# Kernel optimization log

Hardware: AMD Instinct MI355X
Metric: run time of the kernel (lower is better)

Reference implementation:

```python
import jax, jax.numpy as jnp
import numpy as np

N_NODES = 50000
N_EDGES = 800000
IN_C, OUT_C, EDGE_F, HEADS, HID, FINAL = 8, 16, 8, 4, 64, 128
NEG_SLOPE = 0.2  # PyG GATConv default LeakyReLU slope


def setup_inputs() -> dict:
    key = jax.random.key(0)
    ks = jax.random.split(key, 12)
    s = 0.1
    return {
        "x": jax.random.normal(ks[0], (N_NODES, IN_C), jnp.float32),
        "edge_index": jax.random.randint(ks[1], (2, N_EDGES), 0, N_NODES, jnp.int64),
        "edge_attr": jax.random.normal(ks[2], (N_EDGES, EDGE_F), jnp.float32),
        # NNConv params: root weight, bias, edge-MLP Linear(EDGE_F -> IN_C*OUT_C)
        "ecc_root": jax.random.normal(ks[3], (IN_C, OUT_C), jnp.float32) * s,
        "ecc_bias": jnp.zeros((OUT_C,), jnp.float32),
        "mlp_w": jax.random.normal(ks[4], (EDGE_F, IN_C * OUT_C), jnp.float32) * s,
        "mlp_b": jnp.zeros((IN_C * OUT_C,), jnp.float32),
        # GATConv params
        "gat_lin": jax.random.normal(ks[5], (OUT_C, HEADS * HID), jnp.float32) * s,
        "att_src": jax.random.normal(ks[6], (HEADS, HID), jnp.float32) * s,
        "att_dst": jax.random.normal(ks[7], (HEADS, HID), jnp.float32) * s,
        "gat_bias": jnp.zeros((HEADS * HID,), jnp.float32),
        # final Linear
        "fc_w": jax.random.normal(ks[8], (HEADS * HID, FINAL), jnp.float32) * s,
        "fc_b": jnp.zeros((FINAL,), jnp.float32),
    }


def _forward(x, edge_index, edge_attr, ecc_root, ecc_bias, mlp_w, mlp_b,
             gat_lin, att_src, att_dst, gat_bias, fc_w, fc_b):
    src, dst = edge_index[0], edge_index[1]  # messages flow src -> dst

    # ---- NNConv (edge-conditioned conv), aggr='add' ----
    # per-edge weight matrices [E, IN_C, OUT_C] from edge MLP
    w_e = (edge_attr @ mlp_w + mlp_b).reshape(-1, IN_C, OUT_C)
    msg = jnp.einsum('ei,eio->eo', x[src], w_e)                 # [E, OUT_C]
    agg = jax.ops.segment_sum(msg, dst, num_segments=N_NODES)   # [N, OUT_C]
    h = jax.nn.relu(x @ ecc_root + agg + ecc_bias)              # [N, OUT_C]

    # ---- GATConv (heads concatenated) ----
    g = (h @ gat_lin).reshape(N_NODES, HEADS, HID)              # [N, H, D]
    a_src = jnp.einsum('nhd,hd->nh', g, att_src)                # [N, H]
    a_dst = jnp.einsum('nhd,hd->nh', g, att_dst)
    e = jax.nn.leaky_relu(a_src[src] + a_dst[dst], NEG_SLOPE)   # [E, H]
    # segment softmax over incoming edges of each dst node
    e_max = jax.ops.segment_max(e, dst, num_segments=N_NODES)   # [N, H]
    e_max = jnp.where(jnp.isfinite(e_max), e_max, 0.0)
    e_exp = jnp.exp(e - e_max[dst])                             # [E, H]
    denom = jax.ops.segment_sum(e_exp, dst, num_segments=N_NODES)
    alpha = e_exp / (denom[dst] + 1e-16)                        # [E, H]
    out = jax.ops.segment_sum(alpha[:, :, None] * g[src], dst,
                              num_segments=N_NODES)             # [N, H, D]
    out = jax.nn.relu(out.reshape(N_NODES, HEADS * HID) + gat_bias)

    # ---- final linear ----
    return out @ fc_w + fc_b                                    # [N, FINAL]


def reference(x, edge_index, edge_attr, ecc_root, ecc_bias, mlp_w, mlp_b,
              gat_lin, att_src, att_dst, gat_bias, fc_w, fc_b):
    return _forward(x, edge_index, edge_attr, ecc_root, ecc_bias, mlp_w, mlp_b,
                    gat_lin, att_src, att_dst, gat_bias, fc_w, fc_b)
```

## Files before the change

kernel.cpp:

```cpp
#include <hip/hip_runtime.h>

#define N_NODES 50000
#define N_EDGES 800000
#define IN_C 8
#define OUT_C 16
#define EDGE_F 8
#define HEADS 4
#define HID 64
#define GDIM (HEADS*HID)
#define FINAL 128
#define NEG_SLOPE 0.2f
#define EB ((N_EDGES+255)/256)
#define NBLK 196

__device__ __forceinline__ int clampn(int v) {
    return v < 0 ? 0 : (v >= N_NODES ? N_NODES - 1 : v);
}

__global__ __launch_bounds__(256) void k_histfold(
    const int* __restrict__ dst, int* __restrict__ cnt, int* __restrict__ rnk,
    const float* __restrict__ gat_lin,
    const float* __restrict__ att_src_w, const float* __restrict__ att_dst_w,
    float* __restrict__ wsrc, float* __restrict__ wdst)
{
    if (blockIdx.x < EB) {
        int e = blockIdx.x * 256 + threadIdx.x;
        if (e >= N_EDGES) return;
        rnk[e] = atomicAdd(&cnt[clampn(dst[e])], 1);
    } else {
        int t = threadIdx.x;
        if (t >= 64) return;
        int c = t >> 2, h = t & 3;
        float ws = 0.f, wd = 0.f;
        for (int k = 0; k < HID; k++) {
            float l = gat_lin[c * GDIM + h * HID + k];
            ws += l * att_src_w[h * HID + k];
            wd += l * att_dst_w[h * HID + k];
        }
        wsrc[t] = ws;
        wdst[t] = wd;
    }
}

__global__ __launch_bounds__(256) void k_part(const int* __restrict__ cnt,
                                              int* __restrict__ part)
{
    int i = blockIdx.x * 256 + threadIdx.x;
    int v = (i < N_NODES) ? cnt[i] : 0;
#pragma unroll
    for (int off = 32; off; off >>= 1) v += __shfl_down(v, off);
    __shared__ int ws[4];
    if ((threadIdx.x & 63) == 0) ws[threadIdx.x >> 6] = v;
    __syncthreads();
    if (threadIdx.x == 0) part[blockIdx.x] = ws[0] + ws[1] + ws[2] + ws[3];
}

__global__ __launch_bounds__(256) void k_scan1(const int* __restrict__ part,
                                               int* __restrict__ partscan)
{
    int t = threadIdx.x;
    int v = (t < NBLK) ? part[t] : 0;
    int lane = t & 63, wid = t >> 6;
    int incl = v;
#pragma unroll
    for (int off = 1; off < 64; off <<= 1) {
        int u = __shfl_up(incl, off);
        if (lane >= off) incl += u;
    }
    __shared__ int wsum[4];
    if (lane == 63) wsum[wid] = incl;
    __syncthreads();
    int add = 0;
    for (int w = 0; w < wid; w++) add += wsum[w];
    partscan[t] = incl - v + add;
}

__global__ __launch_bounds__(256) void k_add(const int* __restrict__ cnt,
                                             const int* __restrict__ partscan,
                                             int* __restrict__ offs)
{
    int i = blockIdx.x * 256 + threadIdx.x;
    int v = (i < N_NODES) ? cnt[i] : 0;
    int lane = threadIdx.x & 63, wid = threadIdx.x >> 6;
    int incl = v;
#pragma unroll
    for (int off = 1; off < 64; off <<= 1) {
        int u = __shfl_up(incl, off);
        if (lane >= off) incl += u;
    }
    __shared__ int wsum[4];
    if (lane == 63) wsum[wid] = incl;
    __syncthreads();
    int add = partscan[blockIdx.x];
    for (int w = 0; w < wid; w++) add += wsum[w];
    if (i < N_NODES) offs[i] = incl - v + add;
    if (i == 0) offs[N_NODES] = N_EDGES;
}

__global__ __launch_bounds__(256) void k_scatter(
    const int* __restrict__ src, const int* __restrict__ dst,
    const int* __restrict__ rnk, const int* __restrict__ offs,
    int2* __restrict__ se_csr)
{
    int e = blockIdx.x * 256 + threadIdx.x;
    if (e >= N_EDGES) return;
    int p = offs[clampn(dst[e])] + rnk[e];
    se_csr[p] = make_int2(clampn(src[e]), e);
}

__global__ __launch_bounds__(256) void k2T_wave(
    const float* __restrict__ x,
    const int2* __restrict__ se_csr, const int* __restrict__ offs,
    const float* __restrict__ ea,
    const float* __restrict__ mlp_w, const float* __restrict__ mlp_b,
    const float* __restrict__ ecc_root, const float* __restrict__ ecc_bias,
    const float* __restrict__ wsrc, const float* __restrict__ wdst,
    float* __restrict__ h_tab, float* __restrict__ asrc, float* __restrict__ adst)
{
    __shared__ float smW[64 * 17];
    __shared__ float smb[128];
    __shared__ float sroot[128];
    __shared__ float sbias[16];
    __shared__ float sws[64], swd[64];
    __shared__ float sT[4][64];
    __shared__ float sxs[4][8];

    int t = threadIdx.x;
    for (int idx = t; idx < 1024; idx += 256)
        smW[(idx >> 4) * 17 + (idx & 15)] = mlp_w[idx];
    if (t < 128) smb[t] = mlp_b[t];
    if (t >= 128 && t < 256) sroot[t - 128] = ecc_root[t - 128];
    if (t < 16) sbias[t] = ecc_bias[t];
    if (t >= 32 && t < 96) sws[t - 32] = wsrc[t - 32];
    if (t >= 96 && t < 160) swd[t - 96] = wdst[t - 96];

    int wid = t >> 6, lane = t & 63;
    int n = blockIdx.x * 4 + wid;
    int f = lane >> 3, i = lane & 7;
    int beg = offs[n], end = offs[n + 1];

    float t0 = 0.f, t1 = 0.f, t2 = 0.f, t3 = 0.f, xs = 0.f;
    int j = beg;
    for (; j + 3 < end; j += 4) {
        int2 se0 = se_csr[j],     se1 = se_csr[j + 1];
        int2 se2 = se_csr[j + 2], se3 = se_csr[j + 3];
        float a0 = ea[(size_t)se0.y * EDGE_F + f];
        float a1 = ea[(size_t)se1.y * EDGE_F + f];
        float a2 = ea[(size_t)se2.y * EDGE_F + f];
        float a3 = ea[(size_t)se3.y * EDGE_F + f];
        float x0 = x[se0.x * IN_C + i];
        float x1 = x[se1.x * IN_C + i];
        float x2 = x[se2.x * IN_C + i];
        float x3 = x[se3.x * IN_C + i];
        t0 += a0 * x0; t1 += a1 * x1; t2 += a2 * x2; t3 += a3 * x3;
        xs += (x0 + x1) + (x2 + x3);
    }
    for (; j < end; j++) {
        int2 se = se_csr[j];
        float a = ea[(size_t)se.y * EDGE_F + f];
        float xv = x[se.x * IN_C + i];
        t0 += a * xv;
        xs += xv;
    }
    sT[wid][lane] = (t0 + t1) + (t2 + t3);
    if (f == 0) sxs[wid][i] = xs;
    __syncthreads();

    int o = lane & 15, p = lane >> 4;
    float v = 0.f;
#pragma unroll
    for (int q2 = 0; q2 < 16; q2++) {
        int jj = p * 16 + q2;
        v += smW[jj * 17 + o] * sT[wid][jj];
    }
    v += __shfl_down(v, 32);
    v += __shfl_down(v, 16);

    float hv = 0.f;
    if (lane < 16) {
        float vv = v + sbias[o];
#pragma unroll
        for (int ii = 0; ii < IN_C; ii++) {
            vv += smb[ii * 16 + o] * sxs[wid][ii];
            vv += x[n * IN_C + ii] * sroot[ii * 16 + o];
        }
        hv = fmaxf(vv, 0.f);
        h_tab[n * OUT_C + o] = hv;
    }
    float as = 0.f, ad = 0.f;
    int h2 = lane & 3;
#pragma unroll
    for (int c = 0; c < 16; c++) {
        float hc = __shfl(hv, c);
        as += hc * sws[c * 4 + h2];
        ad += hc * swd[c * 4 + h2];
    }
    if (lane < 4) {
        asrc[n * HEADS + lane] = as;
        adst[n * HEADS + lane] = ad;
    }
}

__global__ __launch_bounds__(256) void k_gatE(
    const int* __restrict__ offs, const int2* __restrict__ se_csr,
    const float* __restrict__ asrc, const float* __restrict__ adst,
    const float* __restrict__ h_tab, float* __restrict__ U_all)
{
    int t = threadIdx.x;
    int wid = t >> 6, lane = t & 63;
    int n = blockIdx.x * 4 + wid;
    int h = lane >> 4, c = lane & 15;
    float adsth = adst[n * HEADS + h];
    int beg = offs[n], end = offs[n + 1];

    float U = 0.f, den = 0.f;
    int j = beg;
    for (; j + 3 < end; j += 4) {
        int s0 = se_csr[j].x,     s1 = se_csr[j + 1].x;
        int s2 = se_csr[j + 2].x, s3 = se_csr[j + 3].x;
        float av0 = asrc[s0 * HEADS + h], av1 = asrc[s1 * HEADS + h];
        float av2 = asrc[s2 * HEADS + h], av3 = asrc[s3 * HEADS + h];
        float h0 = h_tab[s0 * OUT_C + c], h1 = h_tab[s1 * OUT_C + c];
        float h2v = h_tab[s2 * OUT_C + c], h3v = h_tab[s3 * OUT_C + c];
        float v0 = av0 + adsth; v0 = v0 > 0.f ? v0 : NEG_SLOPE * v0;
        float v1 = av1 + adsth; v1 = v1 > 0.f ? v1 : NEG_SLOPE * v1;
        float v2 = av2 + adsth; v2 = v2 > 0.f ? v2 : NEG_SLOPE * v2;
        float v3 = av3 + adsth; v3 = v3 > 0.f ? v3 : NEG_SLOPE * v3;
        float p0 = __expf(v0), p1 = __expf(v1), p2 = __expf(v2), p3 = __expf(v3);
        den += (p0 + p1) + (p2 + p3);
        U += p0 * h0 + p1 * h1 + p2 * h2v + p3 * h3v;
    }
    for (; j < end; j++) {
        int s = se_csr[j].x;
        float av = asrc[s * HEADS + h];
        float hvv = h_tab[s * OUT_C + c];
        float v = av + adsth; v = v > 0.f ? v : NEG_SLOPE * v;
        float pe = __expf(v);
        den += pe;
        U += pe * hvv;
    }
    U_all[(size_t)n * 64 + lane] = U / (den + 1e-16f);
}

#define FBM 32
__global__ __launch_bounds__(256, 5) void k_fuse(
    const float* __restrict__ U_all, const float* __restrict__ gat_lin,
    const float* __restrict__ gat_bias, const float* __restrict__ fc_w,
    const float* __restrict__ fc_b, float* __restrict__ y)
{
    __shared__ float slin[16 * GDIM];
    __shared__ float sA[16][FBM + 4];
    __shared__ float sW[16][FINAL];
    int tid = threadIdx.x;
    int r0 = blockIdx.x * FBM;

    for (int idx = tid; idx < (16 * GDIM) / 4; idx += 256)
        ((float4*)slin)[idx] = ((const float4*)gat_lin)[idx];
    __syncthreads();

    int ar  = tid >> 3;
    int ak  = (tid & 7) * 2;
    int grow = r0 + ar;

    int tcol = (tid & 31) * 4;
    int trow = (tid >> 5) * 4;

    float acc[4][4];
#pragma unroll
    for (int r = 0; r < 4; r++)
#pragma unroll
        for (int c = 0; c < 4; c++) acc[r][c] = 0.f;

    for (int h = 0; h < HEADS; ++h) {
        float4 ua = make_float4(0.f, 0.f, 0.f, 0.f), ub = ua, uc4 = ua, ud = ua;
        if (grow < N_NODES) {
            const float4* up = (const float4*)&U_all[(size_t)grow * 64 + h * 16];
            ua = up[0]; ub = up[1]; uc4 = up[2]; ud = up[3];
        }
        float ureg[16] = {ua.x, ua.y, ua.z, ua.w,  ub.x, ub.y, ub.z, ub.w,
                          uc4.x, uc4.y, uc4.z, uc4.w,  ud.x, ud.y, ud.z, ud.w};

#pragma unroll
        for (int tt = 0; tt < 4; ++tt) {
            int k0 = h * 64 + tt * 16;
            float b0 = gat_bias[k0 + ak];
            float b1 = gat_bias[k0 + ak + 1];
            float g0 = 0.f, g1 = 0.f;
#pragma unroll
            for (int c = 0; c < 16; ++c) {
                const float* lp = &slin[c * GDIM + k0 + ak];
                g0 += ureg[c] * lp[0];
                g1 += ureg[c] * lp[1];
            }
            __syncthreads();
            sA[ak][ar]     = fmaxf(g0 + b0, 0.f);
            sA[ak + 1][ar] = fmaxf(g1 + b1, 0.f);
#pragma unroll
            for (int p = 0; p < 2; ++p) {
                int kk = (tid >> 5) + p * 8;
                int cc = (tid & 31) * 4;
                *(float4*)&sW[kk][cc] =
                    *(const float4*)&fc_w[(size_t)(k0 + kk) * FINAL + cc];
            }
            __syncthreads();
#pragma unroll
            for (int kk = 0; kk < 16; ++kk) {
                float4 w = *(const float4*)&sW[kk][tcol];
                float4 a = *(const float4*)&sA[kk][trow];
                float av[4] = {a.x, a.y, a.z, a.w};
#pragma unroll
                for (int r = 0; r < 4; r++) {
                    acc[r][0] += av[r] * w.x;
                    acc[r][1] += av[r] * w.y;
                    acc[r][2] += av[r] * w.z;
                    acc[r][3] += av[r] * w.w;
                }
            }
        }
    }

    float4 fb = *(const float4*)&fc_b[tcol];
#pragma unroll
    for (int r = 0; r < 4; r++) {
        int row = r0 + trow + r;
        if (row < N_NODES) {
            *(float4*)&y[(size_t)row * FINAL + tcol] =
                make_float4(acc[r][0] + fb.x, acc[r][1] + fb.y,
                            acc[r][2] + fb.z, acc[r][3] + fb.w);
        }
    }
}

extern "C" void kernel_launch(void* const* d_in, const int* in_sizes, int n_in,
                              void* d_out, int out_size, void* d_ws, size_t ws_size,
                              hipStream_t stream)
{
    const float* x        = (const float*)d_in[0];
    const int*   ei       = (const int*)d_in[1];
    const float* ea       = (const float*)d_in[2];
    const float* ecc_root = (const float*)d_in[3];
    const float* ecc_bias = (const float*)d_in[4];
    const float* mlp_w    = (const float*)d_in[5];
    const float* mlp_b    = (const float*)d_in[6];
    const float* gat_lin  = (const float*)d_in[7];
    const float* att_src  = (const float*)d_in[8];
    const float* att_dst  = (const float*)d_in[9];
    const float* gat_bias = (const float*)d_in[10];
    const float* fc_w     = (const float*)d_in[11];
    const float* fc_b     = (const float*)d_in[12];
    float* y = (float*)d_out;

    const int* src = ei;
    const int* dst = ei + N_EDGES;

    float* h_tab = (float*)d_ws;
    float* U_all = h_tab + (size_t)N_NODES * OUT_C;
    float* asrc  = U_all + (size_t)N_NODES * 64;
    float* adst  = asrc + (size_t)N_NODES * HEADS;
    float* wsrc  = adst + (size_t)N_NODES * HEADS;
    float* wdst  = wsrc + 64;
    int*   cnt      = (int*)(wdst + 64);
    int*   offs     = cnt + N_NODES;
    int*   part     = offs + N_NODES + 1;
    int*   partscan = part + 256;
    int*   rnk      = partscan + 256;
    int2*  se_csr   = (int2*)(rnk + N_EDGES + 1);

    hipMemsetAsync(cnt, 0, sizeof(int) * N_NODES, stream);

    k_histfold<<<EB + 1, 256, 0, stream>>>(dst, cnt, rnk, gat_lin, att_src, att_dst,
                                           wsrc, wdst);
    k_part    <<<NBLK, 256, 0, stream>>>(cnt, part);
    k_scan1   <<<1, 256, 0, stream>>>(part, partscan);
    k_add     <<<NBLK, 256, 0, stream>>>(cnt, partscan, offs);
    k_scatter <<<EB, 256, 0, stream>>>(src, dst, rnk, offs, se_csr);

    k2T_wave  <<<N_NODES / 4, 256, 0, stream>>>(x, se_csr, offs, ea, mlp_w, mlp_b,
                                                ecc_root, ecc_bias, wsrc, wdst,
                                                h_tab, asrc, adst);
    k_gatE    <<<N_NODES / 4, 256, 0, stream>>>(offs, se_csr, asrc, adst, h_tab, U_all);
    k_fuse    <<<(N_NODES + FBM - 1) / FBM, 256, 0, stream>>>(U_all, gat_lin, gat_bias,
                                                              fc_w, fc_b, y);
}
```

Baseline: 316.3 us.

## Permute edge attributes into CSR order and split fc_w reads between LDS and global

The scatter kernel now writes a separate src index array plus a copy of edge_attr permuted into dst-sorted CSR order. The edge-conditioned aggregation can then read edge features contiguously instead of gathering them by edge id. k_fuse drops the shared copy of gat_lin and reads it from global/cache, and stages only half of fc_w in LDS while the other waves read fc_w directly from global memory. The aim is to cut random gathers and LDS footprint so occupancy rises, at the cost of extra scatter write traffic and more global reads in the fused GEMM.

```diff
diff --git a/kernel.cpp b/kernel.cpp
--- a/kernel.cpp
+++ b/kernel.cpp
@@ -100,18 +100,23 @@
 __global__ __launch_bounds__(256) void k_scatter(
     const int* __restrict__ src, const int* __restrict__ dst,
     const int* __restrict__ rnk, const int* __restrict__ offs,
-    int2* __restrict__ se_csr)
+    const float* __restrict__ ea,
+    int* __restrict__ src_csr, float* __restrict__ ea_csr)
 {
     int e = blockIdx.x * 256 + threadIdx.x;
     if (e >= N_EDGES) return;
     int p = offs[clampn(dst[e])] + rnk[e];
-    se_csr[p] = make_int2(clampn(src[e]), e);
+    src_csr[p] = clampn(src[e]);
+    const float4* s4 = (const float4*)&ea[(size_t)e * EDGE_F];
+    float4* d4 = (float4*)&ea_csr[(size_t)p * EDGE_F];
+    d4[0] = s4[0];
+    d4[1] = s4[1];
 }
 
 __global__ __launch_bounds__(256) void k2T_wave(
     const float* __restrict__ x,
-    const int2* __restrict__ se_csr, const int* __restrict__ offs,
-    const float* __restrict__ ea,
+    const int* __restrict__ src_csr, const int* __restrict__ offs,
+    const float* __restrict__ ea_csr,
     const float* __restrict__ mlp_w, const float* __restrict__ mlp_b,
     const float* __restrict__ ecc_root, const float* __restrict__ ecc_bias,
     const float* __restrict__ wsrc, const float* __restrict__ wdst,
@@ -142,23 +147,23 @@
     float t0 = 0.f, t1 = 0.f, t2 = 0.f, t3 = 0.f, xs = 0.f;
     int j = beg;
     for (; j + 3 < end; j += 4) {
-        int2 se0 = se_csr[j],     se1 = se_csr[j + 1];
-        int2 se2 = se_csr[j + 2], se3 = se_csr[j + 3];
-        float a0 = ea[(size_t)se0.y * EDGE_F + f];
-        float a1 = ea[(size_t)se1.y * EDGE_F + f];
-        float a2 = ea[(size_t)se2.y * EDGE_F + f];
-        float a3 = ea[(size_t)se3.y * EDGE_F + f];
-        float x0 = x[se0.x * IN_C + i];
-        float x1 = x[se1.x * IN_C + i];
-        float x2 = x[se2.x * IN_C + i];
-        float x3 = x[se3.x * IN_C + i];
+        int s0 = src_csr[j],     s1 = src_csr[j + 1];
+        int s2 = src_csr[j + 2], s3 = src_csr[j + 3];
+        float a0 = ea_csr[(size_t)j * EDGE_F + f];
+        float a1 = ea_csr[(size_t)(j + 1) * EDGE_F + f];
+        float a2 = ea_csr[(size_t)(j + 2) * EDGE_F + f];
+        float a3 = ea_csr[(size_t)(j + 3) * EDGE_F + f];
+        float x0 = x[s0 * IN_C + i];
+        float x1 = x[s1 * IN_C + i];
+        float x2 = x[s2 * IN_C + i];
+        float x3 = x[s3 * IN_C + i];
         t0 += a0 * x0; t1 += a1 * x1; t2 += a2 * x2; t3 += a3 * x3;
         xs += (x0 + x1) + (x2 + x3);
     }
     for (; j < end; j++) {
-        int2 se = se_csr[j];
-        float a = ea[(size_t)se.y * EDGE_F + f];
-        float xv = x[se.x * IN_C + i];
+        int s = src_csr[j];
+        float a = ea_csr[(size_t)j * EDGE_F + f];
+        float xv = x[s * IN_C + i];
         t0 += a * xv;
         xs += xv;
     }
@@ -202,7 +207,7 @@
 }
 
 __global__ __launch_bounds__(256) void k_gatE(
-    const int* __restrict__ offs, const int2* __restrict__ se_csr,
+    const int* __restrict__ offs, const int* __restrict__ src_csr,
     const float* __restrict__ asrc, const float* __restrict__ adst,
     const float* __restrict__ h_tab, float* __restrict__ U_all)
 {
@@ -216,8 +221,8 @@
     float U = 0.f, den = 0.f;
     int j = beg;
     for (; j + 3 < end; j += 4) {
-        int s0 = se_csr[j].x,     s1 = se_csr[j + 1].x;
-        int s2 = se_csr[j + 2].x, s3 = se_csr[j + 3].x;
+        int s0 = src_csr[j],     s1 = src_csr[j + 1];
+        int s2 = src_csr[j + 2], s3 = src_csr[j + 3];
         float av0 = asrc[s0 * HEADS + h], av1 = asrc[s1 * HEADS + h];
         float av2 = asrc[s2 * HEADS + h], av3 = asrc[s3 * HEADS + h];
         float h0 = h_tab[s0 * OUT_C + c], h1 = h_tab[s1 * OUT_C + c];
@@ -231,7 +236,7 @@
         U += p0 * h0 + p1 * h1 + p2 * h2v + p3 * h3v;
     }
     for (; j < end; j++) {
-        int s = se_csr[j].x;
+        int s = src_csr[j];
         float av = asrc[s * HEADS + h];
         float hvv = h_tab[s * OUT_C + c];
         float v = av + adsth; v = v > 0.f ? v : NEG_SLOPE * v;
@@ -243,27 +248,28 @@
 }
 
 #define FBM 32
-__global__ __launch_bounds__(256, 5) void k_fuse(
+__global__ __launch_bounds__(256) void k_fuse(
     const float* __restrict__ U_all, const float* __restrict__ gat_lin,
     const float* __restrict__ gat_bias, const float* __restrict__ fc_w,
     const float* __restrict__ fc_b, float* __restrict__ y)
 {
-    __shared__ float slin[16 * GDIM];
     __shared__ float sA[16][FBM + 4];
-    __shared__ float sW[16][FINAL];
+    __shared__ float sW[16][64];
     int tid = threadIdx.x;
     int r0 = blockIdx.x * FBM;
-
-    for (int idx = tid; idx < (16 * GDIM) / 4; idx += 256)
-        ((float4*)slin)[idx] = ((const float4*)gat_lin)[idx];
-    __syncthreads();
 
     int ar  = tid >> 3;
     int ak  = (tid & 7) * 2;
     int grow = r0 + ar;
 
-    int tcol = (tid & 31) * 4;
-    int trow = (tid >> 5) * 4;
+    int w    = tid >> 6;
+    int lane = tid & 63;
+    int trow = (w >> 1) * 16 + (lane >> 4) * 4;
+    int tcol = (w & 1) * 64 + (lane & 15) * 4;
+    bool useLds = ((w & 1) == 0);
+
+    int skk = tid >> 4;
+    int scc = (tid & 15) * 4;
 
     float acc[4][4];
 #pragma unroll
@@ -288,32 +294,44 @@
             float g0 = 0.f, g1 = 0.f;
 #pragma unroll
             for (int c = 0; c < 16; ++c) {
-                const float* lp = &slin[c * GDIM + k0 + ak];
+                const float* lp = &gat_lin[c * GDIM + k0 + ak];
                 g0 += ureg[c] * lp[0];
                 g1 += ureg[c] * lp[1];
             }
             __syncthreads();
             sA[ak][ar]     = fmaxf(g0 + b0, 0.f);
             sA[ak + 1][ar] = fmaxf(g1 + b1, 0.f);
-#pragma unroll
-            for (int p = 0; p < 2; ++p) {
-                int kk = (tid >> 5) + p * 8;
-                int cc = (tid & 31) * 4;
-                *(float4*)&sW[kk][cc] =
-                    *(const float4*)&fc_w[(size_t)(k0 + kk) * FINAL + cc];
-            }
+            *(float4*)&sW[skk][scc] =
+                *(const float4*)&fc_w[(size_t)(k0 + skk) * FINAL + scc];
             __syncthreads();
-#pragma unroll
-            for (int kk = 0; kk < 16; ++kk) {
-                float4 w = *(const float4*)&sW[kk][tcol];
-                float4 a = *(const float4*)&sA[kk][trow];
-                float av[4] = {a.x, a.y, a.z, a.w};
-#pragma unroll
-                for (int r = 0; r < 4; r++) {
-                    acc[r][0] += av[r] * w.x;
-                    acc[r][1] += av[r] * w.y;
-                    acc[r][2] += av[r] * w.z;
-                    acc[r][3] += av[r] * w.w;
+
+            if (useLds) {
+#pragma unroll
+                for (int kk = 0; kk < 16; ++kk) {
+                    float4 wv = *(const float4*)&sW[kk][tcol];
+                    float4 a = *(const float4*)&sA[kk][trow];
+                    float av[4] = {a.x, a.y, a.z, a.w};
+#pragma unroll
+                    for (int r = 0; r < 4; r++) {
+                        acc[r][0] += av[r] * wv.x;
+                        acc[r][1] += av[r] * wv.y;
+                        acc[r][2] += av[r] * wv.z;
+                        acc[r][3] += av[r] * wv.w;
+                    }
+                }
+            } else {
+#pragma unroll
+                for (int kk = 0; kk < 16; ++kk) {
+                    float4 wv = *(const float4*)&fc_w[(size_t)(k0 + kk) * FINAL + tcol];
+                    float4 a = *(const float4*)&sA[kk][trow];
+                    float av[4] = {a.x, a.y, a.z, a.w};
+#pragma unroll
+                    for (int r = 0; r < 4; r++) {
+                        acc[r][0] += av[r] * wv.x;
+                        acc[r][1] += av[r] * wv.y;
+                        acc[r][2] += av[r] * wv.z;
+                        acc[r][3] += av[r] * wv.w;
+                    }
                 }
             }
         }
@@ -361,10 +379,11 @@
     float* wdst  = wsrc + 64;
     int*   cnt      = (int*)(wdst + 64);
     int*   offs     = cnt + N_NODES;
-    int*   part     = offs + N_NODES + 1;
+    int*   part     = offs + N_NODES + 4;
     int*   partscan = part + 256;
     int*   rnk      = partscan + 256;
-    int2*  se_csr   = (int2*)(rnk + N_EDGES + 1);
+    int*   src_csr  = rnk + N_EDGES;
+    float* ea_csr   = (float*)(src_csr + N_EDGES);
 
     hipMemsetAsync(cnt, 0, sizeof(int) * N_NODES, stream);
 
@@ -373,12 +392,12 @@
     k_part    <<<NBLK, 256, 0, stream>>>(cnt, part);
     k_scan1   <<<1, 256, 0, stream>>>(part, partscan);
     k_add     <<<NBLK, 256, 0, stream>>>(cnt, partscan, offs);
-    k_scatter <<<EB, 256, 0, stream>>>(src, dst, rnk, offs, se_csr);
-
-    k2T_wave  <<<N_NODES / 4, 256, 0, stream>>>(x, se_csr, offs, ea, mlp_w, mlp_b,
+    k_scatter <<<EB, 256, 0, stream>>>(src, dst, rnk, offs, ea, src_csr, ea_csr);
+
+    k2T_wave  <<<N_NODES / 4, 256, 0, stream>>>(x, src_csr, offs, ea_csr, mlp_w, mlp_b,
                                                 ecc_root, ecc_bias, wsrc, wdst,
                                                 h_tab, asrc, adst);
-    k_gatE    <<<N_NODES / 4, 256, 0, stream>>>(offs, se_csr, asrc, adst, h_tab, U_all);
+    k_gatE    <<<N_NODES / 4, 256, 0, stream>>>(offs, src_csr, asrc, adst, h_tab, U_all);
     k_fuse    <<<(N_NODES + FBM - 1) / FBM, 256, 0, stream>>>(U_all, gat_lin, gat_bias,
                                                               fc_w, fc_b, y);
 }
```

Measured after the change: 384.1 us. 1.21x slower.

## Double row tile in fused GAT-output/FC kernel with 4x8 per-thread microtile

Applied to the files above, without the earlier changes.

Raises the fused kernel's row tile from 32 to 64 nodes and remaps threads so each computes a 4x8 output microtile with two column halves. Each thread now computes four GAT features per row using float4 shared and bias loads. The aim is to halve how often gat_lin is staged into shared memory and fc_w tiles are reloaded per output row, and to raise FMA work per shared-memory load. In exchange the launch-bounds occupancy hint is dropped and register use rises, which may lower occupancy, and there are half as many blocks.

```diff
diff --git a/kernel.cpp b/kernel.cpp
--- a/kernel.cpp
+++ b/kernel.cpp
@@ -242,8 +242,8 @@
     U_all[(size_t)n * 64 + lane] = U / (den + 1e-16f);
 }
 
-#define FBM 32
-__global__ __launch_bounds__(256, 5) void k_fuse(
+#define FBM 64
+__global__ __launch_bounds__(256) void k_fuse(
     const float* __restrict__ U_all, const float* __restrict__ gat_lin,
     const float* __restrict__ gat_bias, const float* __restrict__ fc_w,
     const float* __restrict__ fc_b, float* __restrict__ y)
@@ -258,18 +258,21 @@
         ((float4*)slin)[idx] = ((const float4*)gat_lin)[idx];
     __syncthreads();
 
-    int ar  = tid >> 3;
-    int ak  = (tid & 7) * 2;
+    int ar  = tid >> 2;
+    int akq = (tid & 3) * 4;
     int grow = r0 + ar;
 
-    int tcol = (tid & 31) * 4;
-    int trow = (tid >> 5) * 4;
-
-    float acc[4][4];
+    int rg = tid >> 4;
+    int cg = tid & 15;
+
+    int skk = tid >> 4;
+    int scc = (tid & 15) * 4;
+
+    float acc[4][8];
 #pragma unroll
     for (int r = 0; r < 4; r++)
 #pragma unroll
-        for (int c = 0; c < 4; c++) acc[r][c] = 0.f;
+        for (int c = 0; c < 8; c++) acc[r][c] = 0.f;
 
     for (int h = 0; h < HEADS; ++h) {
         float4 ua = make_float4(0.f, 0.f, 0.f, 0.f), ub = ua, uc4 = ua, ud = ua;
@@ -283,50 +286,61 @@
 #pragma unroll
         for (int tt = 0; tt < 4; ++tt) {
             int k0 = h * 64 + tt * 16;
-            float b0 = gat_bias[k0 + ak];
-            float b1 = gat_bias[k0 + ak + 1];
-            float g0 = 0.f, g1 = 0.f;
+            float4 bv = *(const float4*)&gat_bias[k0 + akq];
+            float g0 = 0.f, g1 = 0.f, g2 = 0.f, g3 = 0.f;
 #pragma unroll
             for (int c = 0; c < 16; ++c) {
-                const float* lp = &slin[c * GDIM + k0 + ak];
-                g0 += ureg[c] * lp[0];
-                g1 += ureg[c] * lp[1];
+                float4 lv = *(const float4*)&slin[c * GDIM + k0 + akq];
+                g0 += ureg[c] * lv.x;
+                g1 += ureg[c] * lv.y;
+                g2 += ureg[c] * lv.z;
+                g3 += ureg[c] * lv.w;
             }
             __syncthreads();
-            sA[ak][ar]     = fmaxf(g0 + b0, 0.f);
-            sA[ak + 1][ar] = fmaxf(g1 + b1, 0.f);
-#pragma unroll
-            for (int p = 0; p < 2; ++p) {
-                int kk = (tid >> 5) + p * 8;
-                int cc = (tid & 31) * 4;
-                *(float4*)&sW[kk][cc] =
-                    *(const float4*)&fc_w[(size_t)(k0 + kk) * FINAL + cc];
+            sA[akq + 0][ar] = fmaxf(g0 + bv.x, 0.f);
+            sA[akq + 1][ar] = fmaxf(g1 + bv.y, 0.f);
+            sA[akq + 2][ar] = fmaxf(g2 + bv.z, 0.f);
+            sA[akq + 3][ar] = fmaxf(g3 + bv.w, 0.f);
+            {
+                const float* wrow = &fc_w[(size_t)(k0 + skk) * FINAL];
+                *(float4*)&sW[skk][scc]      = *(const float4*)&wrow[scc];
+                *(float4*)&sW[skk][scc + 64] = *(const float4*)&wrow[scc + 64];
             }
             __syncthreads();
 #pragma unroll
             for (int kk = 0; kk < 16; ++kk) {
-                float4 w = *(const float4*)&sW[kk][tcol];
-                float4 a = *(const float4*)&sA[kk][trow];
+                float4 a  = *(const float4*)&sA[kk][rg * 4];
+                float4 w0 = *(const float4*)&sW[kk][cg * 4];
+                float4 w1 = *(const float4*)&sW[kk][cg * 4 + 64];
                 float av[4] = {a.x, a.y, a.z, a.w};
 #pragma unroll
                 for (int r = 0; r < 4; r++) {
-                    acc[r][0] += av[r] * w.x;
-                    acc[r][1] += av[r] * w.y;
-                    acc[r][2] += av[r] * w.z;
-                    acc[r][3] += av[r] * w.w;
+                    acc[r][0] += av[r] * w0.x;
+                    acc[r][1] += av[r] * w0.y;
+                    acc[r][2] += av[r] * w0.z;
+                    acc[r][3] += av[r] * w0.w;
+                    acc[r][4] += av[r] * w1.x;
+                    acc[r][5] += av[r] * w1.y;
+                    acc[r][6] += av[r] * w1.z;
+                    acc[r][7] += av[r] * w1.w;
                 }
             }
         }
     }
 
-    float4 fb = *(const float4*)&fc_b[tcol];
+    float4 fb0 = *(const float4*)&fc_b[cg * 4];
+    float4 fb1 = *(const float4*)&fc_b[cg * 4 + 64];
 #pragma unroll
     for (int r = 0; r < 4; r++) {
-        int row = r0 + trow + r;
+        int row = r0 + rg * 4 + r;
         if (row < N_NODES) {
-            *(float4*)&y[(size_t)row * FINAL + tcol] =
-                make_float4(acc[r][0] + fb.x, acc[r][1] + fb.y,
-                            acc[r][2] + fb.z, acc[r][3] + fb.w);
+            float* yp = &y[(size_t)row * FINAL];
+            *(float4*)&yp[cg * 4] =
+                make_float4(acc[r][0] + fb0.x, acc[r][1] + fb0.y,
+                            acc[r][2] + fb0.z, acc[r][3] + fb0.w);
+            *(float4*)&yp[cg * 4 + 64] =
+                make_float4(acc[r][4] + fb1.x, acc[r][5] + fb1.y,
+                            acc[r][6] + fb1.z, acc[r][7] + fb1.w);
         }
     }
 }
```

Measured after the change: 313.1 us. Within noise of the previous version (-1.0%).
